# Kernel tuning notes

Hardware: AMD Instinct MI355X
Metric: run time of the kernel (lower is better)

The kernel has to match this reference:

```python
import jax, jax.numpy as jnp
import numpy as np

N_NODES = 50000
N_EDGES = 1200000
D_FEAT = 64
HIDDEN = 32


def setup_inputs() -> dict:
    key = jax.random.key(0)
    ks = jax.random.split(key, 9)
    x = jax.random.normal(ks[0], (N_NODES, D_FEAT), dtype=jnp.float32)
    edge_index = jax.random.randint(ks[1], (2, N_EDGES), 0, N_NODES, dtype=jnp.int64)
    u = jax.random.normal(ks[2], (N_NODES,), dtype=jnp.float32)
    d_in = 2 * D_FEAT
    # MLP: Linear(d_in,H) -> relu -> Linear(H,H) -> relu -> Linear(H,1)
    W1 = jax.random.normal(ks[3], (d_in, HIDDEN), dtype=jnp.float32) / np.sqrt(d_in)
    b1 = jnp.zeros((HIDDEN,), dtype=jnp.float32)
    W2 = jax.random.normal(ks[4], (HIDDEN, HIDDEN), dtype=jnp.float32) / np.sqrt(HIDDEN)
    b2 = jnp.zeros((HIDDEN,), dtype=jnp.float32)
    W3 = jax.random.normal(ks[5], (HIDDEN, 1), dtype=jnp.float32) / np.sqrt(HIDDEN)
    b3 = jnp.zeros((1,), dtype=jnp.float32)
    return {"x": x, "edge_index": edge_index, "u": u,
            "W1": W1, "b1": b1, "W2": W2, "b2": b2, "W3": W3, "b3": b3}


def reference(x, edge_index, u, W1, b1, W2, b2, W3, b3):
    row, col = edge_index[0], edge_index[1]
    # gather + concat: [E, 2*D]
    x_edge = jnp.concatenate([x[row], x[col]], axis=-1)
    # per-edge MLP -> scalar weight per edge
    h = jax.nn.relu(x_edge @ W1 + b1)
    h = jax.nn.relu(h @ W2 + b2)
    edge_weight = (h @ W3 + b3)[:, 0]  # [E]
    # spmm: f[i] = sum_{e: row[e]==i} w_e * u[col[e]]
    f = jax.ops.segment_sum(edge_weight * u[col], row, num_segments=x.shape[0])
    return f
```

## Files before the change

kernel.cpp:

```cpp
#include <hip/hip_runtime.h>

#define N_NODES 50000
#define N_EDGES 1200000
#define N_TILES (N_NODES / 16)
#define W1T_STRIDE 72
#define K1_BLOCKS 782

#define N_BUCKETS 196
#define BUCKET_CAP 7168
#define EDGES_PER_BLOCK 1920
#define KA_BLOCKS 625
#define D1_BLOCKS (K1_BLOCKS + KA_BLOCKS)
#define KB_SPLIT 4

typedef __attribute__((ext_vector_type(8))) short short8;
typedef __attribute__((ext_vector_type(4))) float floatx4;

__device__ __forceinline__ unsigned short f32_to_bf16(float f) {
    unsigned int v = __float_as_uint(f);
    unsigned int r = v + 0x7FFFu + ((v >> 16) & 1u);
    return (unsigned short)(r >> 16);
}
__device__ __forceinline__ float bf16_to_f32(unsigned short s) {
    return __uint_as_float(((unsigned int)s) << 16);
}
__device__ __forceinline__ unsigned int pack_bf16x2(float lo, float hi) {
    return (unsigned int)f32_to_bf16(lo) | ((unsigned int)f32_to_bf16(hi) << 16);
}

__global__ __launch_bounds__(256) void fused_pre_bin(
    const float* __restrict__ x, const float* __restrict__ W1,
    const float* __restrict__ b1,
    const int* __restrict__ row, const int* __restrict__ col,
    unsigned short* __restrict__ P1, unsigned short* __restrict__ P2,
    unsigned int* __restrict__ buf, int* __restrict__ cursor,
    float* __restrict__ out)
{
    __shared__ union {
        unsigned short W1t[64 * W1T_STRIDE];
        struct {
            unsigned short rankv[EDGES_PER_BLOCK];
            int hist[N_BUCKETS];
            int base[N_BUCKETS];
        } bin;
    } sh;

    const int tid = threadIdx.x;
    const int bid = blockIdx.x;

    if (bid < K1_BLOCKS) {
        const int gtid = bid * 256 + tid;
        for (int i = gtid; i < N_NODES; i += K1_BLOCKS * 256)
            out[i] = 0.0f;

        for (int e = tid; e < 128 * 32; e += 256) {
            const int kp = e >> 5, jp = e & 31;
            sh.W1t[((kp < 64) ? jp : jp + 32) * W1T_STRIDE + (kp & 63)] =
                f32_to_bf16(W1[e]);
        }
        __syncthreads();

        const int lane = tid & 63;
        const int n = lane & 15;
        const int q = lane >> 4;

        const int tile = bid * 4 + (tid >> 6);
        if (tile >= N_TILES) return;

        short8 bw[4][2];
        #pragma unroll
        for (int G = 0; G < 4; ++G)
            #pragma unroll
            for (int h = 0; h < 2; ++h)
                bw[G][h] = *(const short8*)
                    &sh.W1t[(n + 16 * G) * W1T_STRIDE + h * 32 + q * 8];
        const float bias0 = b1[n], bias1 = b1[n + 16];

        const int node = tile * 16 + n;
        const float4* xp  = (const float4*)(x + (size_t)node * 64 + q * 8);
        const float4 xa = xp[0], xb = xp[1];
        const float4* xp2 = (const float4*)(x + (size_t)node * 64 + 32 + q * 8);
        const float4 xc = xp2[0], xd = xp2[1];

        short8 a0, a1;
        a0[0] = (short)f32_to_bf16(xa.x); a0[1] = (short)f32_to_bf16(xa.y);
        a0[2] = (short)f32_to_bf16(xa.z); a0[3] = (short)f32_to_bf16(xa.w);
        a0[4] = (short)f32_to_bf16(xb.x); a0[5] = (short)f32_to_bf16(xb.y);
        a0[6] = (short)f32_to_bf16(xb.z); a0[7] = (short)f32_to_bf16(xb.w);
        a1[0] = (short)f32_to_bf16(xc.x); a1[1] = (short)f32_to_bf16(xc.y);
        a1[2] = (short)f32_to_bf16(xc.z); a1[3] = (short)f32_to_bf16(xc.w);
        a1[4] = (short)f32_to_bf16(xd.x); a1[5] = (short)f32_to_bf16(xd.y);
        a1[6] = (short)f32_to_bf16(xd.z); a1[7] = (short)f32_to_bf16(xd.w);

        floatx4 acc[4];
        #pragma unroll
        for (int G = 0; G < 4; ++G) {
            const float bi = (G == 0) ? bias0 : (G == 1) ? bias1 : 0.0f;
            acc[G] = (floatx4){bi, bi, bi, bi};
            acc[G] = __builtin_amdgcn_mfma_f32_16x16x32_bf16(a0, bw[G][0], acc[G], 0, 0, 0);
            acc[G] = __builtin_amdgcn_mfma_f32_16x16x32_bf16(a1, bw[G][1], acc[G], 0, 0, 0);
        }
        unsigned int* P1d = (unsigned int*)P1;
        unsigned int* P2d = (unsigned int*)P2;
        #pragma unroll
        for (int r = 0; r < 4; ++r) {
            const int nr = tile * 16 + q * 4 + r;
            P1d[(size_t)nr * 16 + n] = pack_bf16x2(acc[0][r], acc[1][r]);
            P2d[(size_t)nr * 16 + n] = pack_bf16x2(acc[2][r], acc[3][r]);
        }
    } else {
        for (int b = tid; b < N_BUCKETS; b += 256) sh.bin.hist[b] = 0;
        __syncthreads();

        const int blockStart = (bid - K1_BLOCKS) * EDGES_PER_BLOCK;

        for (int i = tid; i < EDGES_PER_BLOCK; i += 256) {
            const int r = row[blockStart + i];
            sh.bin.rankv[i] = (unsigned short)atomicAdd(&sh.bin.hist[r >> 8], 1);
        }
        __syncthreads();

        for (int b = tid; b < N_BUCKETS; b += 256)
            sh.bin.base[b] = atomicAdd(&cursor[b], sh.bin.hist[b]);
        __syncthreads();

        for (int i = tid; i < EDGES_PER_BLOCK; i += 256) {
            const int r = row[blockStart + i];
            const int c = col[blockStart + i];
            const int bin = r >> 8;
            buf[(size_t)bin * BUCKET_CAP + sh.bin.base[bin] + (int)sh.bin.rankv[i]] =
                ((unsigned int)(r & 255) << 24) | (unsigned int)c;
        }
    }
}

__global__ __launch_bounds__(512) void bucket_mlp(
    const float* __restrict__ u,
    const float* __restrict__ W2, const float* __restrict__ b2,
    const float* __restrict__ W3, const float* __restrict__ b3,
    const unsigned short* __restrict__ P1, const unsigned short* __restrict__ P2,
    const unsigned int* __restrict__ buf, const int* __restrict__ cursor,
    float* __restrict__ out)
{
    __shared__ float accs[256];
    const int tid = threadIdx.x;
    if (tid < 256) accs[tid] = 0.0f;

    const int b = blockIdx.x >> 2;
    const int s = blockIdx.x & (KB_SPLIT - 1);

    const int lane = tid & 63;
    const int n = lane & 15;
    const int q = lane >> 4;
    const int wave = tid >> 6;

    short8 bf0, bf1;
    #pragma unroll
    for (int i = 0; i < 8; ++i) {
        const int F = q * 4 + (i >> 1) + 16 * (i & 1);
        bf0[i] = (short)f32_to_bf16(W2[F * 32 + n]);
        bf1[i] = (short)f32_to_bf16(W2[F * 32 + n + 16]);
    }
    const float w3n0 = W3[n], w3n1 = W3[n + 16];
    const float b2n0 = b2[n], b2n1 = b2[n + 16];
    const float bias3 = b3[0];

    __syncthreads();

    const int cnt = cursor[b];
    const unsigned int* bb = buf + (size_t)b * BUCKET_CAP;
    const unsigned short* P1b = P1 + (size_t)b * 256 * 32;
    const int nch = (cnt + 31) >> 5;

    #pragma unroll 1
    for (int ch = s * 8 + wave; ch < nch; ch += KB_SPLIT * 8) {
        const int base0 = ch * 32;

        int rl[2], cI[2];
        #pragma unroll
        for (int t = 0; t < 2; ++t) {
            int e = base0 + t * 16 + n;
            if (e >= cnt) e = cnt - 1;
            const unsigned int ent = bb[e];
            rl[t] = (int)(ent >> 24);
            cI[t] = (int)(ent & 0x1FFFFu);
        }
        int r2 = 0; float u2 = 0.0f;
        if (n < 8) {
            const int eloc = base0 + 16 * (n >> 2) + 4 * q + (n & 3);
            const unsigned int ent2 = bb[(eloc < cnt) ? eloc : 0];
            r2 = (int)(ent2 >> 24);
            u2 = (eloc < cnt) ? u[ent2 & 0x1FFFFu] : 0.0f;
        }
        short8 v1[2], v2[2];
        #pragma unroll
        for (int t = 0; t < 2; ++t) {
            v1[t] = *(const short8*)(P1b + (size_t)rl[t] * 32 + q * 8);
            v2[t] = *(const short8*)(P2 + (size_t)cI[t] * 32 + q * 8);
        }

        float tr[2][4];
        #pragma unroll
        for (int t = 0; t < 2; ++t) {
            short8 a;
            #pragma unroll
            for (int i = 0; i < 8; ++i) {
                const float f1 = bf16_to_f32((unsigned short)v1[t][i]);
                const float f2 = bf16_to_f32((unsigned short)v2[t][i]);
                a[i] = (short)f32_to_bf16(fmaxf(f1 + f2, 0.0f));
            }
            floatx4 d0 = {b2n0, b2n0, b2n0, b2n0};
            floatx4 d1 = {b2n1, b2n1, b2n1, b2n1};
            d0 = __builtin_amdgcn_mfma_f32_16x16x32_bf16(a, bf0, d0, 0, 0, 0);
            d1 = __builtin_amdgcn_mfma_f32_16x16x32_bf16(a, bf1, d1, 0, 0, 0);
            #pragma unroll
            for (int r = 0; r < 4; ++r)
                tr[t][r] = fmaxf(d0[r], 0.0f) * w3n0 + fmaxf(d1[r], 0.0f) * w3n1;
        }

        #pragma unroll
        for (int mask = 1; mask < 16; mask <<= 1) {
            #pragma unroll
            for (int t = 0; t < 2; ++t)
                #pragma unroll
                for (int r = 0; r < 4; ++r)
                    tr[t][r] += __shfl_xor(tr[t][r], mask, 64);
        }

        if (n < 8) {
            const float va0 = (n & 4) ? tr[1][0] : tr[0][0];
            const float va1 = (n & 4) ? tr[1][1] : tr[0][1];
            const float va2 = (n & 4) ? tr[1][2] : tr[0][2];
            const float va3 = (n & 4) ? tr[1][3] : tr[0][3];
            const float vb0 = (n & 2) ? va2 : va0;
            const float vb1 = (n & 2) ? va3 : va1;
            const float v   = (n & 1) ? vb1 : vb0;
            atomicAdd(&accs[r2], (v + bias3) * u2);
        }
    }

    __syncthreads();

    if (tid < 256) {
        const int node = b * 256 + tid;
        if (node < N_NODES) atomicAdd(out + node, accs[tid]);
    }
}

extern "C" void kernel_launch(void* const* d_in, const int* in_sizes, int n_in,
                              void* d_out, int out_size, void* d_ws, size_t ws_size,
                              hipStream_t stream)
{
    const float* x    = (const float*)d_in[0];
    const int*   eidx = (const int*)  d_in[1];
    const float* u    = (const float*)d_in[2];
    const float* W1   = (const float*)d_in[3];
    const float* b1   = (const float*)d_in[4];
    const float* W2   = (const float*)d_in[5];
    const float* b2   = (const float*)d_in[6];
    const float* W3   = (const float*)d_in[7];
    const float* b3   = (const float*)d_in[8];

    const int* row = eidx;
    const int* col = eidx + N_EDGES;

    unsigned short* P1 = (unsigned short*)d_ws;
    unsigned short* P2 = (unsigned short*)((char*)d_ws + (size_t)N_NODES * 64);
    unsigned int*  buf = (unsigned int*)((char*)d_ws + (size_t)N_NODES * 128);
    int* cursor = (int*)((char*)d_ws + (size_t)N_NODES * 128
                         + (size_t)N_BUCKETS * BUCKET_CAP * 4);
    float* out = (float*)d_out;

    hipMemsetAsync(cursor, 0, N_BUCKETS * sizeof(int), stream);

    fused_pre_bin<<<D1_BLOCKS, 256, 0, stream>>>(
        x, W1, b1, row, col, P1, P2, buf, cursor, out);

    bucket_mlp<<<N_BUCKETS * KB_SPLIT, 512, 0, stream>>>(
        u, W2, b2, W3, b3, P1, P2, buf, cursor, out);
}
```

Measured before the change: 135.6 us.

## Software-pipeline edge index loads in bucket MLP and cache row ids in LDS

In the bucket MLP kernel, the loop now loads the next chunk's edge entries and u values while the current chunk's P1/P2 gathers and MFMAs run. This is meant to break the dependent chain of index load, then feature gather, then compute, and so hide global memory latency. In the binning branch, row ids are kept in shared memory as 16-bit values so the second pass does not reload them from global memory. The prefetch adds register pressure, and the ushort cast relies on node ids being below 65536.

```diff
diff --git a/kernel.cpp b/kernel.cpp
--- a/kernel.cpp
+++ b/kernel.cpp
@@ -40,6 +40,7 @@
         unsigned short W1t[64 * W1T_STRIDE];
         struct {
             unsigned short rankv[EDGES_PER_BLOCK];
+            unsigned short rowv[EDGES_PER_BLOCK];
             int hist[N_BUCKETS];
             int base[N_BUCKETS];
         } bin;
@@ -116,6 +117,7 @@
 
         for (int i = tid; i < EDGES_PER_BLOCK; i += 256) {
             const int r = row[blockStart + i];
+            sh.bin.rowv[i]  = (unsigned short)r;
             sh.bin.rankv[i] = (unsigned short)atomicAdd(&sh.bin.hist[r >> 8], 1);
         }
         __syncthreads();
@@ -125,7 +127,7 @@
         __syncthreads();
 
         for (int i = tid; i < EDGES_PER_BLOCK; i += 256) {
-            const int r = row[blockStart + i];
+            const int r = (int)sh.bin.rowv[i];
             const int c = col[blockStart + i];
             const int bin = r >> 8;
             buf[(size_t)bin * BUCKET_CAP + sh.bin.base[bin] + (int)sh.bin.rankv[i]] =
@@ -171,12 +173,14 @@
     const unsigned int* bb = buf + (size_t)b * BUCKET_CAP;
     const unsigned short* P1b = P1 + (size_t)b * 256 * 32;
     const int nch = (cnt + 31) >> 5;
-
-    #pragma unroll 1
-    for (int ch = s * 8 + wave; ch < nch; ch += KB_SPLIT * 8) {
+    const int STRIDE = KB_SPLIT * 8;
+
+    int ch = s * 8 + wave;
+    int rl[2], cI[2];
+    int r2 = 0; float u2 = 0.0f;
+
+    if (ch < nch) {
         const int base0 = ch * 32;
-
-        int rl[2], cI[2];
         #pragma unroll
         for (int t = 0; t < 2; ++t) {
             int e = base0 + t * 16 + n;
@@ -185,18 +189,42 @@
             rl[t] = (int)(ent >> 24);
             cI[t] = (int)(ent & 0x1FFFFu);
         }
-        int r2 = 0; float u2 = 0.0f;
         if (n < 8) {
             const int eloc = base0 + 16 * (n >> 2) + 4 * q + (n & 3);
             const unsigned int ent2 = bb[(eloc < cnt) ? eloc : 0];
             r2 = (int)(ent2 >> 24);
             u2 = (eloc < cnt) ? u[ent2 & 0x1FFFFu] : 0.0f;
         }
+    }
+
+    #pragma unroll 1
+    while (ch < nch) {
         short8 v1[2], v2[2];
         #pragma unroll
         for (int t = 0; t < 2; ++t) {
             v1[t] = *(const short8*)(P1b + (size_t)rl[t] * 32 + q * 8);
             v2[t] = *(const short8*)(P2 + (size_t)cI[t] * 32 + q * 8);
+        }
+
+        const int chn = ch + STRIDE;
+        int nrl[2], ncI[2];
+        int nr2 = 0; float nu2 = 0.0f;
+        if (chn < nch) {
+            const int base1 = chn * 32;
+            #pragma unroll
+            for (int t = 0; t < 2; ++t) {
+                int e = base1 + t * 16 + n;
+                if (e >= cnt) e = cnt - 1;
+                const unsigned int ent = bb[e];
+                nrl[t] = (int)(ent >> 24);
+                ncI[t] = (int)(ent & 0x1FFFFu);
+            }
+            if (n < 8) {
+                const int eloc = base1 + 16 * (n >> 2) + 4 * q + (n & 3);
+                const unsigned int ent2 = bb[(eloc < cnt) ? eloc : 0];
+                nr2 = (int)(ent2 >> 24);
+                nu2 = (eloc < cnt) ? u[ent2 & 0x1FFFFu] : 0.0f;
+            }
         }
 
         float tr[2][4];
@@ -237,6 +265,11 @@
             const float v   = (n & 1) ? vb1 : vb0;
             atomicAdd(&accs[r2], (v + bias3) * u2);
         }
+
+        rl[0] = nrl[0]; rl[1] = nrl[1];
+        cI[0] = ncI[0]; cI[1] = ncI[1];
+        r2 = nr2; u2 = nu2;
+        ch = chn;
     }
 
     __syncthreads();
```

Result: no change. 136.2 us (+0.5%).
